# Performance work log

Measured on AMD Instinct MI355X. Metric: run time of the kernel, lower is better.

The kernel has to match this reference:

```python
import jax, jax.numpy as jnp
import numpy as np

SR = 3            # search_range
K = 5             # template_sz
S = 2 * SR + 1    # search window size (7)
KSZ = 5           # bilateral kernel size
SIG_S = 1.5       # bilateral spatial sigma
SIG_I = 0.05      # bilateral intensity sigma


def _patches(x, k, pad):
    # x: (B,C,H,W) -> (B, C*k*k, H', W'); channel order (C, kh, kw) matches torch unfold
    return jax.lax.conv_general_dilated_patches(x, (k, k), (1, 1), pad)


def _binomial(x):
    # separable [1 2 1]/4 with replicate padding
    xp = jnp.pad(x, ((0, 0), (0, 0), (1, 1), (0, 0)), mode='edge')
    v = (xp[:, :, :-2, :] + 2.0 * x + xp[:, :, 2:, :]) / 4.0
    vp = jnp.pad(v, ((0, 0), (0, 0), (0, 0), (1, 1)), mode='edge')
    return (vp[:, :, :, :-2] + 2.0 * v + vp[:, :, :, 2:]) / 4.0


def _gradient(f):
    fp = jnp.pad(f, ((0, 0), (0, 0), (1, 1), (1, 1)), mode='edge')
    fy = (fp[:, :, 2:, 1:-1] - fp[:, :, :-2, 1:-1]) / 2.0
    fx = (fp[:, :, 1:-1, 2:] - fp[:, :, 1:-1, :-2]) / 2.0
    return fy, fx


def _templates(img):
    # (B,1,H,W) -> (B,H,W,1,K*K)  per-pixel KxK patch (zero SAME padding)
    p = _patches(img, K, [(K // 2, K // 2)] * 2)      # (B,K*K,H,W)
    return jnp.transpose(p, (0, 2, 3, 1))[:, :, :, None, :]


def _search_windows(img):
    # (B,1,H,W) -> (B,H,W,S*S,K*K): KxK templates at every displacement in SxS window
    B, _, H, W = img.shape
    xp = jnp.pad(img, ((0, 0), (0, 0), (SR, SR), (SR, SR)))      # zero pad by max_sr
    p1 = _patches(xp, K, [(K // 2, K // 2)] * 2)                  # (B,K*K,H+2SR,W+2SR)
    p2 = _patches(p1, S, 'VALID')                                 # (B,K*K*S*S,H,W)
    p2 = p2.reshape(B, K * K, S, S, H, W)
    return jnp.transpose(p2, (0, 4, 5, 2, 3, 1)).reshape(B, H, W, S * S, K * K)


def _spiral_rank():
    # rank of each flat (S*S) displacement in a center-out spiral traversal
    sz = S
    order = np.zeros(sz * sz, np.int32)
    j = i = 0
    rank = 0
    order[(j + SR) * sz + (i + SR)] = rank
    rank += 1
    dirs = [(0, 1), (1, 0), (0, -1), (-1, 0)]
    d, step = 0, 1
    while rank < sz * sz:
        for _ in range(2):
            dj, di = dirs[d % 4]
            for _ in range(step):
                j += dj
                i += di
                if abs(j) <= SR and abs(i) <= SR and rank < sz * sz:
                    order[(j + SR) * sz + (i + SR)] = rank
                    rank += 1
            d += 1
        step += 1
    return jnp.asarray(order)


def _subpixel(f_t, g_t, f_img):
    # f_t, g_t: (B,H,W,1,K*K) in 0..255; f_img: (B,1,H,W) float in [0,1]
    f = f_t / 255.0
    g = g_t / 255.0
    dfy_img, dfx_img = _gradient(f_img)
    dfy = _templates(dfy_img)
    dfx = _templates(dfx_img)
    pm = np.zeros((K, K), np.float32)
    pm[0, :] = pm[-1, :] = pm[:, 0] = pm[:, -1] = 1.0   # border ring mask
    pred = jnp.asarray(pm.reshape(-1))
    rs = lambda x: jnp.sum(x, axis=-1, keepdims=True)
    a = rs(dfx * dfx * pred)
    b = rs(dfx * dfy * pred)
    d = rs(dfy * dfy * pred)
    z = g - f
    p = rs(z * dfx * pred)
    q = rs(z * dfy * pred)
    det = a * d - b * b
    u = d * p - b * q
    v = a * q - b * p
    sub = jnp.concatenate([v, u], axis=-1)              # (B,H,W,1,2) (y,x)
    det_bad = det <= 1e-7
    sub = sub / jnp.where(det_bad, 1.0, det)            # safe divide; masked anyway
    sub = jnp.where(det_bad | (jnp.abs(sub) >= 1.0), 0.0, sub)
    return jnp.transpose(sub[:, :, :, 0, :], (0, 3, 1, 2))   # (B,2,H,W)


def _median3(x):
    # 3x3 median with replicate (SYMMETRIC) padding
    B, C, H, W = x.shape
    xp = jnp.pad(x, ((0, 0), (0, 0), (1, 1), (1, 1)), mode='edge')
    p = _patches(xp, 3, 'VALID').reshape(B, C, 9, H, W)
    return jnp.sort(p, axis=2)[:, :, 4]


def _bilateral(t, vec):
    # t: (B,1,H,W) guide; vec: (B,2,H,W) flow
    B, _, H, W = t.shape
    k2 = KSZ * KSZ
    kernel = -1.0 / (2.0 * SIG_S ** 2) * jnp.ones((k2,), jnp.float32)
    sii = 1.0 / (2.0 * SIG_I ** 2)
    cp = jnp.transpose(t, (0, 2, 3, 1))[:, :, :, None, :]                # (B,H,W,1,1)
    ck = jnp.transpose(_patches(t, KSZ, [(KSZ // 2, KSZ // 2)] * 2).reshape(B, 1, k2, H, W), (0, 3, 4, 2, 1))  # (B,H,W,k2,1)
    idiff = jnp.sum((cp - ck) ** 2, axis=-1)                             # (B,H,W,k2)
    coeff = jnp.clip(1.0 - jnp.abs(kernel - idiff * sii), 0.0, 1.0)[..., None]
    vb = jnp.transpose(_patches(vec, KSZ, [(KSZ // 2, KSZ // 2)] * 2).reshape(B, 2, k2, H, W), (0, 3, 4, 2, 1))  # (B,H,W,k2,2)
    out = jnp.sum(vb * coeff, axis=-2) / jnp.sum(coeff, axis=-2)
    return jnp.transpose(out, (0, 3, 1, 2))


def setup_inputs() -> dict:
    key = jax.random.key(0)
    k1, k2 = jax.random.split(key)
    H = W = 256
    f_img = jax.random.uniform(k1, (1, 1, H, W), jnp.float32)
    g_img = jax.random.uniform(k2, (1, 1, H, W), jnp.float32)
    return {'f_img': f_img, 'g_img': g_img}


def reference(f_img, g_img):
    fb = _binomial(f_img)
    gb = _binomial(g_img)
    # quantize to uint8-valued floats (matches _cast float->uint8)
    fq = jnp.clip(jnp.round(fb * 255.0), 0.0, 255.0)
    gq = jnp.clip(jnp.round(gb * 255.0), 0.0, 255.0)
    w1 = _search_windows(fq)                 # (B,H,W,S*S,K*K)
    w2 = _templates(gq)                      # (B,H,W,1,K*K)
    cost = jnp.sum(jnp.abs(w1 - w2), axis=-1).astype(jnp.int32)   # (B,H,W,S*S)
    rank = _spiral_rank()
    score = cost * 64 + rank                 # lexicographic (cost, spiral rank); rank < 64
    idx = jnp.argmin(score, axis=-1)         # (B,H,W) spiral-centered argmin
    rng = jnp.arange(-SR, SR + 1, dtype=jnp.float32)
    jj, ii = jnp.meshgrid(rng, rng, indexing='ij')
    vecLUT = -jnp.stack([jj, ii], axis=-1).reshape(-1, 2)
    vector = jnp.transpose(vecLUT[idx], (0, 3, 1, 2))             # (B,2,H,W)
    min_t = jnp.take_along_axis(w1, idx[:, :, :, None, None], axis=3)  # (B,H,W,1,K*K)
    sub = _subpixel(min_t, w2, fb)
    flow = vector + sub
    flow = _median3(flow)
    flow = _bilateral(fb, flow)
    return flow
```

## Files before the change

### kernel.cpp

```cpp
#include <hip/hip_runtime.h>
#include <math.h>

#define H 256
#define W 256
#define TS 16

#if __has_builtin(__builtin_amdgcn_alignbyte)
__device__ __forceinline__ unsigned align_b(unsigned hi, unsigned lo, int sh) {
    return __builtin_amdgcn_alignbyte(hi, lo, sh);
}
#else
__device__ __forceinline__ unsigned align_b(unsigned hi, unsigned lo, int sh) {
    unsigned d;
    asm("v_alignbyte_b32 %0, %1, %2, %3" : "=v"(d) : "v"(hi), "v"(lo), "v"(sh));
    return d;
}
#endif

#if __has_builtin(__builtin_amdgcn_sad_u8)
__device__ __forceinline__ unsigned sad_u8(unsigned a, unsigned b, unsigned acc) {
    return __builtin_amdgcn_sad_u8(a, b, acc);
}
#else
__device__ __forceinline__ unsigned sad_u8(unsigned a, unsigned b, unsigned acc) {
    unsigned d;
    asm("v_sad_u8 %0, %1, %2, %3" : "=v"(d) : "v"(a), "v"(b), "v"(acc));
    return d;
}
#endif

__global__ void k_binq(const float* __restrict__ f, const float* __restrict__ g,
                       float* __restrict__ fb,
                       unsigned char* __restrict__ fq, unsigned char* __restrict__ gq) {
    int x = blockIdx.x * blockDim.x + threadIdx.x;
    int y = blockIdx.y * blockDim.y + threadIdx.y;
    if (x >= W || y >= H) return;
    int ym = max(y - 1, 0), yp = min(y + 1, H - 1);
    int xm = max(x - 1, 0), xp = min(x + 1, W - 1);

    float fvm = (f[ym*W+xm] + 2.0f*f[y*W+xm] + f[yp*W+xm]) * 0.25f;
    float fv0 = (f[ym*W+x ] + 2.0f*f[y*W+x ] + f[yp*W+x ]) * 0.25f;
    float fvp = (f[ym*W+xp] + 2.0f*f[y*W+xp] + f[yp*W+xp]) * 0.25f;
    float fbv = (fvm + 2.0f*fv0 + fvp) * 0.25f;

    float gvm = (g[ym*W+xm] + 2.0f*g[y*W+xm] + g[yp*W+xm]) * 0.25f;
    float gv0 = (g[ym*W+x ] + 2.0f*g[y*W+x ] + g[yp*W+x ]) * 0.25f;
    float gvp = (g[ym*W+xp] + 2.0f*g[y*W+xp] + g[yp*W+xp]) * 0.25f;
    float gbv = (gvm + 2.0f*gv0 + gvp) * 0.25f;

    fb[y*W+x] = fbv;
    fq[y*W+x] = (unsigned char)fminf(fmaxf(rintf(fbv * 255.0f), 0.0f), 255.0f);
    gq[y*W+x] = (unsigned char)fminf(fmaxf(rintf(gbv * 255.0f), 0.0f), 255.0f);
}

__global__ void __launch_bounds__(256)
k_search(const unsigned char* __restrict__ fq, const unsigned char* __restrict__ gq,
         const float* __restrict__ fb, float* __restrict__ flow) {
    __shared__ unsigned sfq[26 * 7];
    __shared__ unsigned sgq[20 * 5];
    __shared__ float    sfb[22 * 22];

    int tx = threadIdx.x, ty = threadIdx.y;
    int bx0 = blockIdx.x * TS, by0 = blockIdx.y * TS;
    int tid = ty * TS + tx;

    unsigned char* sfq_b = (unsigned char*)sfq;
    unsigned char* sgq_b = (unsigned char*)sgq;

    for (int i = tid; i < 26 * 28; i += 256) {
        int r = i / 28, c = i % 28;
        int gy = by0 + r - 5, gx = bx0 + c - 5;
        sfq_b[i] = (gy >= 0 && gy < H && gx >= 0 && gx < W) ? fq[gy*W+gx] : 0;
    }
    for (int i = tid; i < 20 * 20; i += 256) {
        int r = i / 20, c = i % 20;
        int gy = by0 + r - 2, gx = bx0 + c - 2;
        sgq_b[r * 20 + c] = (gy >= 0 && gy < H && gx >= 0 && gx < W) ? gq[gy*W+gx] : 0;
    }
    for (int i = tid; i < 22 * 22; i += 256) {
        int r = i / 22, c = i % 22;
        int gy = min(max(by0 + r - 3, 0), H - 1);
        int gx = min(max(bx0 + c - 3, 0), W - 1);
        sfb[i] = fb[gy*W+gx];
    }
    __syncthreads();

    int x = bx0 + tx, y = by0 + ty;
    int base = tx >> 2, a = tx & 3;

    unsigned w0[11], w1[11], w2[11];
    #pragma unroll
    for (int r = 0; r < 11; r++) {
        const unsigned* row = &sfq[(ty + r) * 7 + base];
        unsigned d0 = row[0], d1 = row[1], d2 = row[2], d3 = row[3];
        w0[r] = align_b(d1, d0, a);
        w1[r] = align_b(d2, d1, a);
        w2[r] = align_b(d3, d2, a);
    }

    unsigned gt_lo[5], gt_hi[5];
    #pragma unroll
    for (int r = 0; r < 5; r++) {
        const unsigned* row = &sgq[(ty + r) * 5 + base];
        unsigned d0 = row[0], d1 = row[1];
        gt_lo[r] = align_b(d1, d0, a);
        gt_hi[r] = (d1 >> (8 * a)) & 0xFFu;
    }

    const unsigned RANKC[49] = {
        42,43,44,45,46,47,48,
        41,20,21,22,23,24,25,
        40,19, 6, 7, 8, 9,26,
        39,18, 5, 0, 1,10,27,
        38,17, 4, 3, 2,11,28,
        37,16,15,14,13,12,29,
        36,35,34,33,32,31,30
    };

    unsigned best = 0xFFFFFFFFu;
    int bestd = 0;
    #pragma unroll
    for (int si = 0; si < 7; si++) {
        unsigned fd[11], f5[11];
        #pragma unroll
        for (int r = 0; r < 11; r++) {
            fd[r] = (si < 4) ? align_b(w1[r], w0[r], si) : align_b(w2[r], w1[r], si - 4);
            f5[r] = (si < 4) ? ((w1[r] >> (8 * si)) & 0xFFu)
                             : ((w2[r] >> (8 * (si - 4))) & 0xFFu);
        }
        #pragma unroll
        for (int sj = 0; sj < 7; sj++) {
            unsigned acc0 = 0, acc1 = 0;
            #pragma unroll
            for (int kh = 0; kh < 5; kh++) {
                acc0 = sad_u8(fd[sj + kh], gt_lo[kh], acc0);
                acc1 = sad_u8(f5[sj + kh], gt_hi[kh], acc1);
            }
            unsigned score = ((acc0 + acc1) << 6) + RANKC[sj * 7 + si];
            if (score < best) { best = score; bestd = sj * 7 + si; }
        }
    }
    int dy = bestd / 7 - 3, dx = bestd % 7 - 3;

    float aA = 0.f, bB = 0.f, dD = 0.f, pP = 0.f, qQ = 0.f;
    #pragma unroll
    for (int kh = 0; kh < 5; kh++) {
        #pragma unroll
        for (int kw = 0; kw < 5; kw++) {
            if (kh != 0 && kh != 4 && kw != 0 && kw != 4) continue;
            int yy = y + kh - 2, xx = x + kw - 2;
            if (yy < 0 || yy >= H || xx < 0 || xx >= W) continue;
            int ry = ty + kh + 1, rx = tx + kw + 1;
            float gxv = (sfb[ry*22 + rx+1] - sfb[ry*22 + rx-1]) * 0.5f;
            float gyv = (sfb[(ry+1)*22 + rx] - sfb[(ry-1)*22 + rx]) * 0.5f;
            float fv = (float)sfq_b[(ty + dy + kh + 3) * 28 + (tx + dx + kw + 3)] * (1.0f/255.0f);
            float gv = (float)((kw < 4) ? ((gt_lo[kh] >> (8*kw)) & 0xFFu) : gt_hi[kh]) * (1.0f/255.0f);
            float z = gv - fv;
            aA += gxv * gxv;
            bB += gxv * gyv;
            dD += gyv * gyv;
            pP += z * gxv;
            qQ += z * gyv;
        }
    }
    float det = aA * dD - bB * bB;
    float u = dD * pP - bB * qQ;
    float v = aA * qQ - bB * pP;
    float suby = 0.f, subx = 0.f;
    if (det > 1e-7f) {
        suby = v / det;
        subx = u / det;
        if (fabsf(suby) >= 1.0f) suby = 0.f;
        if (fabsf(subx) >= 1.0f) subx = 0.f;
    }
    flow[y*W + x]       = (float)(-dy) + suby;
    flow[H*W + y*W + x] = (float)(-dx) + subx;
}

__global__ void __launch_bounds__(256)
k_medbil(const float* __restrict__ flow1, const float* __restrict__ fb,
         float* __restrict__ out) {
    __shared__ float sfl[2][22 * 22];
    __shared__ float smed[2][20 * 20];
    __shared__ float sfbt[20 * 20];

    int tx = threadIdx.x, ty = threadIdx.y;
    int bx0 = blockIdx.x * TS, by0 = blockIdx.y * TS;
    int tid = ty * TS + tx;

    for (int i = tid; i < 2 * 22 * 22; i += 256) {
        int c = i / 484, rem = i % 484;
        int r = rem / 22, col = rem % 22;
        int qy = min(max(by0 + r - 3, 0), H - 1);
        int qx = min(max(bx0 + col - 3, 0), W - 1);
        sfl[c][rem] = flow1[c*H*W + qy*W + qx];
    }
    for (int i = tid; i < 20 * 20; i += 256) {
        int r = i / 20, col = i % 20;
        int yy = by0 + r - 2, xx = bx0 + col - 2;
        sfbt[i] = (yy >= 0 && yy < H && xx >= 0 && xx < W) ? fb[yy*W+xx] : 0.0f;
    }
    __syncthreads();

    for (int i = tid; i < 2 * 20 * 20; i += 256) {
        int c = i / 400, rem = i % 400;
        int r = rem / 20, col = rem % 20;
        int py = by0 + r - 2, px = bx0 + col - 2;
        float m = 0.0f;
        if (py >= 0 && py < H && px >= 0 && px < W) {
            float v[9];
            int n = 0;
            #pragma unroll
            for (int j = 0; j < 3; j++)
                #pragma unroll
                for (int ii = 0; ii < 3; ii++)
                    v[n++] = sfl[c][(r + j) * 22 + (col + ii)];
#define MSWAP(A, B) { float t_ = fminf(v[A], v[B]); v[B] = fmaxf(v[A], v[B]); v[A] = t_; }
            MSWAP(1,2); MSWAP(4,5); MSWAP(7,8);
            MSWAP(0,1); MSWAP(3,4); MSWAP(6,7);
            MSWAP(1,2); MSWAP(4,5); MSWAP(7,8);
            MSWAP(0,3); MSWAP(5,8); MSWAP(4,7);
            MSWAP(3,6); MSWAP(1,4); MSWAP(2,5);
            MSWAP(4,7); MSWAP(4,2); MSWAP(6,4);
            MSWAP(4,2);
#undef MSWAP
            m = v[4];
        }
        smed[c][rem] = m;
    }
    __syncthreads();

    int x = bx0 + tx, y = by0 + ty;
    const float kern = -0.22222222222222221f;
    const float sii  = 200.0f;
    float cp = sfbt[(ty + 2) * 20 + (tx + 2)];
    float sc = 0.f, sy = 0.f, sx = 0.f;
    #pragma unroll
    for (int j = 0; j < 5; j++) {
        #pragma unroll
        for (int i = 0; i < 5; i++) {
            int s = (ty + j) * 20 + (tx + i);
            float ck = sfbt[s];
            float df = cp - ck;
            float coeff = 1.0f - fabsf(kern - df * df * sii);
            coeff = fminf(fmaxf(coeff, 0.0f), 1.0f);
            sc += coeff;
            sy += coeff * smed[0][s];
            sx += coeff * smed[1][s];
        }
    }
    out[y*W + x]       = sy / sc;
    out[H*W + y*W + x] = sx / sc;
}

extern "C" void kernel_launch(void* const* d_in, const int* in_sizes, int n_in,
                              void* d_out, int out_size, void* d_ws, size_t ws_size,
                              hipStream_t stream) {
    const float* f = (const float*)d_in[0];
    const float* g = (const float*)d_in[1];
    float* out = (float*)d_out;

    char* ws = (char*)d_ws;
    float*         fb    = (float*)(ws);
    unsigned char* fq    = (unsigned char*)(ws + 262144);
    unsigned char* gq    = (unsigned char*)(ws + 327680);
    float*         flow1 = (float*)(ws + 393216);

    dim3 blk(TS, TS);
    dim3 grd(W / TS, H / TS);
    k_binq  <<<grd, blk, 0, stream>>>(f, g, fb, fq, gq);
    k_search<<<grd, blk, 0, stream>>>(fq, gq, fb, flow1);
    k_medbil<<<grd, blk, 0, stream>>>(flow1, fb, out);
}
```

Measured before the change: 67.57 us.

## Fuse blur, block-matching search, median and bilateral into one kernel

```diff
diff --git a/kernel.cpp b/kernel.cpp
--- a/kernel.cpp
+++ b/kernel.cpp
@@ -29,83 +29,87 @@
 }
 #endif
 
-__global__ void k_binq(const float* __restrict__ f, const float* __restrict__ g,
-                       float* __restrict__ fb,
-                       unsigned char* __restrict__ fq, unsigned char* __restrict__ gq) {
-    int x = blockIdx.x * blockDim.x + threadIdx.x;
-    int y = blockIdx.y * blockDim.y + threadIdx.y;
-    if (x >= W || y >= H) return;
-    int ym = max(y - 1, 0), yp = min(y + 1, H - 1);
-    int xm = max(x - 1, 0), xp = min(x + 1, W - 1);
-
-    float fvm = (f[ym*W+xm] + 2.0f*f[y*W+xm] + f[yp*W+xm]) * 0.25f;
-    float fv0 = (f[ym*W+x ] + 2.0f*f[y*W+x ] + f[yp*W+x ]) * 0.25f;
-    float fvp = (f[ym*W+xp] + 2.0f*f[y*W+xp] + f[yp*W+xp]) * 0.25f;
-    float fbv = (fvm + 2.0f*fv0 + fvp) * 0.25f;
-
-    float gvm = (g[ym*W+xm] + 2.0f*g[y*W+xm] + g[yp*W+xm]) * 0.25f;
-    float gv0 = (g[ym*W+x ] + 2.0f*g[y*W+x ] + g[yp*W+x ]) * 0.25f;
-    float gvp = (g[ym*W+xp] + 2.0f*g[y*W+xp] + g[yp*W+xp]) * 0.25f;
-    float gbv = (gvm + 2.0f*gv0 + gvp) * 0.25f;
-
-    fb[y*W+x] = fbv;
-    fq[y*W+x] = (unsigned char)fminf(fmaxf(rintf(fbv * 255.0f), 0.0f), 255.0f);
-    gq[y*W+x] = (unsigned char)fminf(fmaxf(rintf(gbv * 255.0f), 0.0f), 255.0f);
+__device__ __forceinline__ float binom3x3(const float* s, int r, int c, int stride) {
+    float vm = (s[(r-1)*stride + (c-1)] + 2.0f*s[r*stride + (c-1)] + s[(r+1)*stride + (c-1)]) * 0.25f;
+    float v0 = (s[(r-1)*stride + (c  )] + 2.0f*s[r*stride + (c  )] + s[(r+1)*stride + (c  )]) * 0.25f;
+    float vp = (s[(r-1)*stride + (c+1)] + 2.0f*s[r*stride + (c+1)] + s[(r+1)*stride + (c+1)]) * 0.25f;
+    return (vm + 2.0f*v0 + vp) * 0.25f;
+}
+
+__device__ __forceinline__ unsigned quant255(float v) {
+    return (unsigned)fminf(fmaxf(rintf(v * 255.0f), 0.0f), 255.0f);
 }
 
 __global__ void __launch_bounds__(256)
-k_search(const unsigned char* __restrict__ fq, const unsigned char* __restrict__ gq,
-         const float* __restrict__ fb, float* __restrict__ flow) {
-    __shared__ unsigned sfq[26 * 7];
-    __shared__ unsigned sgq[20 * 5];
-    __shared__ float    sfb[22 * 22];
+k_flow_fused(const float* __restrict__ f, const float* __restrict__ g,
+             float* __restrict__ out) {
+    __shared__ float    sf[36 * 36];
+    __shared__ float    sg[28 * 28];
+    __shared__ float    sfb[34 * 35];
+    __shared__ unsigned sfq[34 * 9];
+    __shared__ unsigned sgq[26 * 7];
+    __shared__ float    sflow[2][22 * 22];
+    __shared__ float    smed[2][20 * 20];
 
     int tx = threadIdx.x, ty = threadIdx.y;
     int bx0 = blockIdx.x * TS, by0 = blockIdx.y * TS;
     int tid = ty * TS + tx;
 
-    unsigned char* sfq_b = (unsigned char*)sfq;
-    unsigned char* sgq_b = (unsigned char*)sgq;
-
-    for (int i = tid; i < 26 * 28; i += 256) {
+    for (int i = tid; i < 36 * 36; i += 256) {
+        int r = i / 36, c = i % 36;
+        int gy = min(max(by0 + r - 10, 0), H - 1);
+        int gx = min(max(bx0 + c - 10, 0), W - 1);
+        sf[i] = f[gy * W + gx];
+    }
+    for (int i = tid; i < 28 * 28; i += 256) {
         int r = i / 28, c = i % 28;
-        int gy = by0 + r - 5, gx = bx0 + c - 5;
-        sfq_b[i] = (gy >= 0 && gy < H && gx >= 0 && gx < W) ? fq[gy*W+gx] : 0;
-    }
-    for (int i = tid; i < 20 * 20; i += 256) {
-        int r = i / 20, c = i % 20;
-        int gy = by0 + r - 2, gx = bx0 + c - 2;
-        sgq_b[r * 20 + c] = (gy >= 0 && gy < H && gx >= 0 && gx < W) ? gq[gy*W+gx] : 0;
-    }
-    for (int i = tid; i < 22 * 22; i += 256) {
-        int r = i / 22, c = i % 22;
-        int gy = min(max(by0 + r - 3, 0), H - 1);
-        int gx = min(max(bx0 + c - 3, 0), W - 1);
-        sfb[i] = fb[gy*W+gx];
-    }
-    __syncthreads();
-
-    int x = bx0 + tx, y = by0 + ty;
-    int base = tx >> 2, a = tx & 3;
-
-    unsigned w0[11], w1[11], w2[11];
-    #pragma unroll
-    for (int r = 0; r < 11; r++) {
-        const unsigned* row = &sfq[(ty + r) * 7 + base];
-        unsigned d0 = row[0], d1 = row[1], d2 = row[2], d3 = row[3];
-        w0[r] = align_b(d1, d0, a);
-        w1[r] = align_b(d2, d1, a);
-        w2[r] = align_b(d3, d2, a);
-    }
-
-    unsigned gt_lo[5], gt_hi[5];
-    #pragma unroll
-    for (int r = 0; r < 5; r++) {
-        const unsigned* row = &sgq[(ty + r) * 5 + base];
-        unsigned d0 = row[0], d1 = row[1];
-        gt_lo[r] = align_b(d1, d0, a);
-        gt_hi[r] = (d1 >> (8 * a)) & 0xFFu;
-    }
+        int gy = min(max(by0 + r - 6, 0), H - 1);
+        int gx = min(max(bx0 + c - 6, 0), W - 1);
+        sg[i] = g[gy * W + gx];
+    }
+    __syncthreads();
+
+    for (int i = tid; i < 306 + 182; i += 256) {
+        if (i < 306) {
+            int row = i / 9, dw = i % 9;
+            unsigned pack = 0;
+            #pragma unroll
+            for (int b = 0; b < 4; b++) {
+                int col = dw * 4 + b;
+                unsigned q = 0;
+                if (col < 34) {
+                    float bv = 0.0f;
+                    int gy = by0 + row - 9, gx = bx0 + col - 9;
+                    if (gy >= 0 && gy < H && gx >= 0 && gx < W) {
+                        bv = binom3x3(sf, row + 1, col + 1, 36);
+                        q = quant255(bv);
+                    }
+                    sfb[row * 35 + col] = bv;
+                }
+                pack |= q << (8 * b);
+            }
+            sfq[i] = pack;
+        } else {
+            int j = i - 306;
+            int row = j / 7, dw = j % 7;
+            unsigned pack = 0;
+            #pragma unroll
+            for (int b = 0; b < 4; b++) {
+                int col = dw * 4 + b;
+                unsigned q = 0;
+                if (col < 26) {
+                    int gy = by0 + row - 5, gx = bx0 + col - 5;
+                    if (gy >= 0 && gy < H && gx >= 0 && gx < W)
+                        q = quant255(binom3x3(sg, row + 1, col + 1, 28));
+                }
+                pack |= q << (8 * b);
+            }
+            sgq[j] = pack;
+        }
+    }
+    __syncthreads();
+
+    const unsigned char* sfq_b = (const unsigned char*)sfq;
 
     const unsigned RANKC[49] = {
         42,43,44,45,46,47,48,
@@ -117,104 +121,115 @@
         36,35,34,33,32,31,30
     };
 
-    unsigned best = 0xFFFFFFFFu;
-    int bestd = 0;
-    #pragma unroll
-    for (int si = 0; si < 7; si++) {
-        unsigned fd[11], f5[11];
-        #pragma unroll
-        for (int r = 0; r < 11; r++) {
-            fd[r] = (si < 4) ? align_b(w1[r], w0[r], si) : align_b(w2[r], w1[r], si - 4);
-            f5[r] = (si < 4) ? ((w1[r] >> (8 * si)) & 0xFFu)
-                             : ((w2[r] >> (8 * (si - 4))) & 0xFFu);
-        }
-        #pragma unroll
-        for (int sj = 0; sj < 7; sj++) {
-            unsigned acc0 = 0, acc1 = 0;
-            #pragma unroll
-            for (int kh = 0; kh < 5; kh++) {
-                acc0 = sad_u8(fd[sj + kh], gt_lo[kh], acc0);
-                acc1 = sad_u8(f5[sj + kh], gt_hi[kh], acc1);
-            }
-            unsigned score = ((acc0 + acc1) << 6) + RANKC[sj * 7 + si];
-            if (score < best) { best = score; bestd = sj * 7 + si; }
-        }
-    }
-    int dy = bestd / 7 - 3, dx = bestd % 7 - 3;
-
-    float aA = 0.f, bB = 0.f, dD = 0.f, pP = 0.f, qQ = 0.f;
-    #pragma unroll
-    for (int kh = 0; kh < 5; kh++) {
-        #pragma unroll
-        for (int kw = 0; kw < 5; kw++) {
-            if (kh != 0 && kh != 4 && kw != 0 && kw != 4) continue;
-            int yy = y + kh - 2, xx = x + kw - 2;
-            if (yy < 0 || yy >= H || xx < 0 || xx >= W) continue;
-            int ry = ty + kh + 1, rx = tx + kw + 1;
-            float gxv = (sfb[ry*22 + rx+1] - sfb[ry*22 + rx-1]) * 0.5f;
-            float gyv = (sfb[(ry+1)*22 + rx] - sfb[(ry-1)*22 + rx]) * 0.5f;
-            float fv = (float)sfq_b[(ty + dy + kh + 3) * 28 + (tx + dx + kw + 3)] * (1.0f/255.0f);
-            float gv = (float)((kw < 4) ? ((gt_lo[kh] >> (8*kw)) & 0xFFu) : gt_hi[kh]) * (1.0f/255.0f);
-            float z = gv - fv;
-            aA += gxv * gxv;
-            bB += gxv * gyv;
-            dD += gyv * gyv;
-            pP += z * gxv;
-            qQ += z * gyv;
-        }
-    }
-    float det = aA * dD - bB * bB;
-    float u = dD * pP - bB * qQ;
-    float v = aA * qQ - bB * pP;
-    float suby = 0.f, subx = 0.f;
-    if (det > 1e-7f) {
-        suby = v / det;
-        subx = u / det;
-        if (fabsf(suby) >= 1.0f) suby = 0.f;
-        if (fabsf(subx) >= 1.0f) subx = 0.f;
-    }
-    flow[y*W + x]       = (float)(-dy) + suby;
-    flow[H*W + y*W + x] = (float)(-dx) + subx;
-}
-
-__global__ void __launch_bounds__(256)
-k_medbil(const float* __restrict__ flow1, const float* __restrict__ fb,
-         float* __restrict__ out) {
-    __shared__ float sfl[2][22 * 22];
-    __shared__ float smed[2][20 * 20];
-    __shared__ float sfbt[20 * 20];
-
-    int tx = threadIdx.x, ty = threadIdx.y;
-    int bx0 = blockIdx.x * TS, by0 = blockIdx.y * TS;
-    int tid = ty * TS + tx;
-
-    for (int i = tid; i < 2 * 22 * 22; i += 256) {
-        int c = i / 484, rem = i % 484;
-        int r = rem / 22, col = rem % 22;
-        int qy = min(max(by0 + r - 3, 0), H - 1);
-        int qx = min(max(bx0 + col - 3, 0), W - 1);
-        sfl[c][rem] = flow1[c*H*W + qy*W + qx];
-    }
-    for (int i = tid; i < 20 * 20; i += 256) {
-        int r = i / 20, col = i % 20;
-        int yy = by0 + r - 2, xx = bx0 + col - 2;
-        sfbt[i] = (yy >= 0 && yy < H && xx >= 0 && xx < W) ? fb[yy*W+xx] : 0.0f;
+    for (int it = tid; it < 22 * 22; it += 256) {
+        int r = it / 22, c = it % 22;
+        int py = min(max(by0 + r - 3, 0), H - 1);
+        int px = min(max(bx0 + c - 3, 0), W - 1);
+        int ro = py - by0 + 9, co = px - bx0 + 9;
+        int base = (co - 5) >> 2, a = (co - 5) & 3;
+
+        unsigned w0[11], w1[11], w2[11];
+        #pragma unroll
+        for (int r2 = 0; r2 < 11; r2++) {
+            const unsigned* row = &sfq[(ro - 5 + r2) * 9 + base];
+            unsigned d0 = row[0], d1 = row[1], d2 = row[2], d3 = row[3];
+            w0[r2] = align_b(d1, d0, a);
+            w1[r2] = align_b(d2, d1, a);
+            w2[r2] = align_b(d3, d2, a);
+        }
+
+        int gro = py - by0 + 5, gco = px - bx0 + 5;
+        int gbase = (gco - 2) >> 2, ga = (gco - 2) & 3;
+        unsigned gt_lo[5], gt_hi[5];
+        #pragma unroll
+        for (int kh = 0; kh < 5; kh++) {
+            const unsigned* row = &sgq[(gro - 2 + kh) * 7 + gbase];
+            unsigned d0 = row[0], d1 = row[1];
+            gt_lo[kh] = align_b(d1, d0, ga);
+            gt_hi[kh] = (d1 >> (8 * ga)) & 0xFFu;
+        }
+
+        unsigned best = 0xFFFFFFFFu;
+        int bestd = 0;
+        #pragma unroll
+        for (int si = 0; si < 7; si++) {
+            unsigned fd[11], f5[11];
+            #pragma unroll
+            for (int r2 = 0; r2 < 11; r2++) {
+                fd[r2] = (si < 4) ? align_b(w1[r2], w0[r2], si) : align_b(w2[r2], w1[r2], si - 4);
+                f5[r2] = (si < 4) ? ((w1[r2] >> (8 * si)) & 0xFFu)
+                                  : ((w2[r2] >> (8 * (si - 4))) & 0xFFu);
+            }
+            #pragma unroll
+            for (int sj = 0; sj < 7; sj++) {
+                unsigned acc0 = 0, acc1 = 0;
+                #pragma unroll
+                for (int kh = 0; kh < 5; kh++) {
+                    acc0 = sad_u8(fd[sj + kh], gt_lo[kh], acc0);
+                    acc1 = sad_u8(f5[sj + kh], gt_hi[kh], acc1);
+                }
+                unsigned score = ((acc0 + acc1) << 6) + RANKC[sj * 7 + si];
+                if (score < best) { best = score; bestd = sj * 7 + si; }
+            }
+        }
+        int dy = bestd / 7 - 3, dx = bestd % 7 - 3;
+
+        float aA = 0.f, bB = 0.f, dD = 0.f, pP = 0.f, qQ = 0.f;
+        #pragma unroll
+        for (int kh = 0; kh < 5; kh++) {
+            #pragma unroll
+            for (int kw = 0; kw < 5; kw++) {
+                if (kh != 0 && kh != 4 && kw != 0 && kw != 4) continue;
+                int yy = py + kh - 2, xx = px + kw - 2;
+                if (yy < 0 || yy >= H || xx < 0 || xx >= W) continue;
+                int fy = yy - by0 + 9;
+                int fx = xx - bx0 + 9;
+                int xl = max(xx - 1, 0) - bx0 + 9, xr = min(xx + 1, W - 1) - bx0 + 9;
+                int yu = max(yy - 1, 0) - by0 + 9, yd = min(yy + 1, H - 1) - by0 + 9;
+                float gxv = (sfb[fy * 35 + xr] - sfb[fy * 35 + xl]) * 0.5f;
+                float gyv = (sfb[yd * 35 + fx] - sfb[yu * 35 + fx]) * 0.5f;
+                float fv = (float)sfq_b[(ro + dy + kh - 2) * 36 + (co + dx + kw - 2)] * (1.0f / 255.0f);
+                float gv = (float)((kw < 4) ? ((gt_lo[kh] >> (8 * kw)) & 0xFFu) : gt_hi[kh]) * (1.0f / 255.0f);
+                float z = gv - fv;
+                aA += gxv * gxv;
+                bB += gxv * gyv;
+                dD += gyv * gyv;
+                pP += z * gxv;
+                qQ += z * gyv;
+            }
+        }
+        float det = aA * dD - bB * bB;
+        float u = dD * pP - bB * qQ;
+        float v = aA * qQ - bB * pP;
+        float suby = 0.f, subx = 0.f;
+        if (det > 1e-7f) {
+            suby = v / det;
+            subx = u / det;
+            if (fabsf(suby) >= 1.0f) suby = 0.f;
+            if (fabsf(subx) >= 1.0f) subx = 0.f;
+        }
+        sflow[0][it] = (float)(-dy) + suby;
+        sflow[1][it] = (float)(-dx) + subx;
     }
     __syncthreads();
 
     for (int i = tid; i < 2 * 20 * 20; i += 256) {
-        int c = i / 400, rem = i % 400;
-        int r = rem / 20, col = rem % 20;
-        int py = by0 + r - 2, px = bx0 + col - 2;
+        int ch = i / 400, rem = i % 400;
+        int rm = rem / 20, cm = rem % 20;
+        int my = by0 + rm - 2, mx = bx0 + cm - 2;
         float m = 0.0f;
-        if (py >= 0 && py < H && px >= 0 && px < W) {
+        if (my >= 0 && my < H && mx >= 0 && mx < W) {
             float v[9];
             int n = 0;
             #pragma unroll
-            for (int j = 0; j < 3; j++)
+            for (int dj = -1; dj <= 1; dj++) {
                 #pragma unroll
-                for (int ii = 0; ii < 3; ii++)
-                    v[n++] = sfl[c][(r + j) * 22 + (col + ii)];
+                for (int di = -1; di <= 1; di++) {
+                    int fr = min(max(my + dj, 0), H - 1) - by0 + 3;
+                    int fc = min(max(mx + di, 0), W - 1) - bx0 + 3;
+                    v[n++] = sflow[ch][fr * 22 + fc];
+                }
+            }
 #define MSWAP(A, B) { float t_ = fminf(v[A], v[B]); v[B] = fmaxf(v[A], v[B]); v[A] = t_; }
             MSWAP(1,2); MSWAP(4,5); MSWAP(7,8);
             MSWAP(0,1); MSWAP(3,4); MSWAP(6,7);
@@ -226,31 +241,31 @@
 #undef MSWAP
             m = v[4];
         }
-        smed[c][rem] = m;
+        smed[ch][i % 400] = m;
     }
     __syncthreads();
 
     int x = bx0 + tx, y = by0 + ty;
     const float kern = -0.22222222222222221f;
     const float sii  = 200.0f;
-    float cp = sfbt[(ty + 2) * 20 + (tx + 2)];
+    float cp = sfb[(ty + 9) * 35 + (tx + 9)];
     float sc = 0.f, sy = 0.f, sx = 0.f;
     #pragma unroll
     for (int j = 0; j < 5; j++) {
         #pragma unroll
         for (int i = 0; i < 5; i++) {
-            int s = (ty + j) * 20 + (tx + i);
-            float ck = sfbt[s];
+            float ck = sfb[(ty + 7 + j) * 35 + (tx + 7 + i)];
             float df = cp - ck;
             float coeff = 1.0f - fabsf(kern - df * df * sii);
             coeff = fminf(fmaxf(coeff, 0.0f), 1.0f);
+            int s = (ty + j) * 20 + (tx + i);
             sc += coeff;
             sy += coeff * smed[0][s];
             sx += coeff * smed[1][s];
         }
     }
-    out[y*W + x]       = sy / sc;
-    out[H*W + y*W + x] = sx / sc;
+    out[y * W + x]         = sy / sc;
+    out[H * W + y * W + x] = sx / sc;
 }
 
 extern "C" void kernel_launch(void* const* d_in, const int* in_sizes, int n_in,
@@ -259,16 +274,9 @@
     const float* f = (const float*)d_in[0];
     const float* g = (const float*)d_in[1];
     float* out = (float*)d_out;
-
-    char* ws = (char*)d_ws;
-    float*         fb    = (float*)(ws);
-    unsigned char* fq    = (unsigned char*)(ws + 262144);
-    unsigned char* gq    = (unsigned char*)(ws + 327680);
-    float*         flow1 = (float*)(ws + 393216);
+    (void)d_ws; (void)ws_size;
 
     dim3 blk(TS, TS);
     dim3 grd(W / TS, H / TS);
-    k_binq  <<<grd, blk, 0, stream>>>(f, g, fb, fq, gq);
-    k_search<<<grd, blk, 0, stream>>>(fq, gq, fb, flow1);
-    k_medbil<<<grd, blk, 0, stream>>>(flow1, fb, out);
-}
+    k_flow_fused<<<grd, blk, 0, stream>>>(f, g, out);
+}
```

New measurement: 67.99 us. About the same (+0.6%).
